# Performance work log

Hardware: AMD Instinct MI355X
Metric: run time of the kernel (lower is better)

Reference implementation:

```python
import jax, jax.numpy as jnp
import numpy as np

B, D_IN, D_H, D_OUT = 65536, 512, 512, 512
E, N_GATE, G_H = 8, 128, 128


def _glorot(key, shape):
    bound = np.sqrt(6.0 / np.prod(shape[-2:]))
    return jax.random.uniform(key, shape, jnp.float32, -bound, bound)


def setup_inputs() -> dict:
    key = jax.random.key(0)
    ks = jax.random.split(key, 10)
    inp = {
        "z": jax.random.normal(ks[0], (B, D_IN), jnp.float32),
        "idx": jnp.arange(N_GATE, dtype=jnp.int64),
        # gating MLP (nn.Linear stored as [in, out])
        "Wg1": _glorot(ks[1], (N_GATE, G_H)), "bg1": jnp.zeros((G_H,), jnp.float32),
        "Wg2": _glorot(ks[2], (G_H, G_H)), "bg2": jnp.zeros((G_H,), jnp.float32),
        "Wg3": _glorot(ks[3], (G_H, E)), "bg3": jnp.zeros((E,), jnp.float32),
        # expert layers: W [E, in, out], b [E, out]
        "W1": _glorot(ks[4], (E, D_IN, D_H)), "b1": jnp.zeros((E, D_H), jnp.float32),
        "W2": _glorot(ks[5], (E, D_H, D_H)), "b2": jnp.zeros((E, D_H), jnp.float32),
        "W3": _glorot(ks[6], (E, D_H, D_OUT)), "b3": jnp.zeros((E, D_OUT), jnp.float32),
    }
    return inp


def _expert_layer(x, w, W, b):
    # y = sum_e w[:,e] * (x @ W[e] + b[e])  -- soft dense MoE combine
    return jnp.einsum('be,bi,eio->bo', w, x, W) + w @ b


def reference(z, idx, Wg1, bg1, Wg2, bg2, Wg3, bg3, W1, b1, W2, b2, W3, b3):
    # gating MLP on selected features (eval mode: dropout is identity)
    g = jax.nn.elu(z[:, idx] @ Wg1 + bg1)
    g = jax.nn.elu(g @ Wg2 + bg2)
    w = g @ Wg3 + bg3  # raw logits, no softmax (faithful to source)
    # experts encoder
    h = jax.nn.elu(_expert_layer(z, w, W1, b1))
    h = jax.nn.elu(_expert_layer(h, w, W2, b2))
    return _expert_layer(h, w, W3, b3)
```

## Files before the change

kernel.cpp:

```cpp
#include <hip/hip_runtime.h>

#define B_ROWS 65536

typedef __attribute__((ext_vector_type(8))) __bf16 bf16x8;
typedef __attribute__((ext_vector_type(8))) _Float16 f16x8;
typedef __attribute__((ext_vector_type(4))) float f32x4;
typedef __attribute__((ext_vector_type(8))) unsigned short u16x8;

__device__ __forceinline__ unsigned short f2bf(float f) {
  unsigned int u = __float_as_uint(f);
  u += 0x7fffu + ((u >> 16) & 1u);
  return (unsigned short)(u >> 16);
}

__device__ __forceinline__ float elu_f(float v) {
  return v > 0.f ? v : __expf(v) - 1.f;
}

__device__ __forceinline__ void async_ld16(const void* g, void* l) {
  __builtin_amdgcn_global_load_lds(
      (const __attribute__((address_space(1))) void*)g,
      (__attribute__((address_space(3))) void*)l, 16, 0, 0);
}

#define GP 136

__global__ __launch_bounds__(256) void gating_mfma(
    const float* __restrict__ z, const int* __restrict__ idx,
    const float* __restrict__ Wg1, const float* __restrict__ bg1,
    const float* __restrict__ Wg2, const float* __restrict__ bg2,
    const float* __restrict__ Wg3, const float* __restrict__ bg3,
    float* __restrict__ wq, unsigned short* __restrict__ zb) {
  __shared__ _Float16 Ab[128 * GP];
  __shared__ _Float16 Wb[128 * GP];
  __shared__ int idx_l[128];

  const int tid = threadIdx.x;
  const int lane = tid & 63, wave = tid >> 6;
  const int wr = wave >> 1, wc = wave & 1;
  const int lhi = lane >> 4, llo = lane & 15;
  const size_t row0 = (size_t)blockIdx.x * 128;

  if (tid < 128) idx_l[tid] = idx[tid];
  for (int i = tid; i < 16384; i += 256) {
    const int k = i >> 7, n = i & 127;
    Wb[n * GP + k] = (_Float16)Wg1[i];
  }
  {
    const float* zr = z + row0 * 512;
    unsigned short* zo = zb + row0 * 512;
    for (int i = tid; i < 8192; i += 256) {
      const size_t off = (size_t)i * 8;
      float4 a = *(const float4*)(zr + off);
      float4 b = *(const float4*)(zr + off + 4);
      u16x8 r;
      r[0] = f2bf(a.x); r[1] = f2bf(a.y); r[2] = f2bf(a.z); r[3] = f2bf(a.w);
      r[4] = f2bf(b.x); r[5] = f2bf(b.y); r[6] = f2bf(b.z); r[7] = f2bf(b.w);
      *(u16x8*)(zo + off) = r;
    }
  }
  __syncthreads();
  for (int i = tid; i < 16384; i += 256) {
    const int r = i >> 7, c = i & 127;
    Ab[r * GP + c] = (_Float16)z[(row0 + r) * 512 + idx_l[c]];
  }
  __syncthreads();

  const f32x4 vzero = {0.f, 0.f, 0.f, 0.f};

  f32x4 C[4][4];
#pragma unroll
  for (int i = 0; i < 4; i++)
#pragma unroll
    for (int j = 0; j < 4; j++) C[i][j] = vzero;
#pragma unroll
  for (int ks = 0; ks < 4; ks++) {
    f16x8 av[4], bv[4];
#pragma unroll
    for (int fm = 0; fm < 4; fm++)
      av[fm] = *(const f16x8*)&Ab[(wr * 64 + fm * 16 + llo) * GP + ks * 32 + lhi * 8];
#pragma unroll
    for (int fn = 0; fn < 4; fn++)
      bv[fn] = *(const f16x8*)&Wb[(wc * 64 + fn * 16 + llo) * GP + ks * 32 + lhi * 8];
#pragma unroll
    for (int fm = 0; fm < 4; fm++)
#pragma unroll
      for (int fn = 0; fn < 4; fn++)
        C[fm][fn] = __builtin_amdgcn_mfma_f32_16x16x32_f16(av[fm], bv[fn], C[fm][fn], 0, 0, 0);
  }
  __syncthreads();
#pragma unroll
  for (int fm = 0; fm < 4; fm++)
#pragma unroll
    for (int fn = 0; fn < 4; fn++) {
      const int col = wc * 64 + fn * 16 + llo;
      const float bb = bg1[col];
#pragma unroll
      for (int r = 0; r < 4; r++) {
        const int row = wr * 64 + fm * 16 + lhi * 4 + r;
        Ab[row * GP + col] = (_Float16)elu_f(C[fm][fn][r] + bb);
      }
    }
  for (int i = tid; i < 16384; i += 256) {
    const int k = i >> 7, n = i & 127;
    Wb[n * GP + k] = (_Float16)Wg2[i];
  }
  __syncthreads();

#pragma unroll
  for (int i = 0; i < 4; i++)
#pragma unroll
    for (int j = 0; j < 4; j++) C[i][j] = vzero;
#pragma unroll
  for (int ks = 0; ks < 4; ks++) {
    f16x8 av[4], bv[4];
#pragma unroll
    for (int fm = 0; fm < 4; fm++)
      av[fm] = *(const f16x8*)&Ab[(wr * 64 + fm * 16 + llo) * GP + ks * 32 + lhi * 8];
#pragma unroll
    for (int fn = 0; fn < 4; fn++)
      bv[fn] = *(const f16x8*)&Wb[(wc * 64 + fn * 16 + llo) * GP + ks * 32 + lhi * 8];
#pragma unroll
    for (int fm = 0; fm < 4; fm++)
#pragma unroll
      for (int fn = 0; fn < 4; fn++)
        C[fm][fn] = __builtin_amdgcn_mfma_f32_16x16x32_f16(av[fm], bv[fn], C[fm][fn], 0, 0, 0);
  }
  __syncthreads();
#pragma unroll
  for (int fm = 0; fm < 4; fm++)
#pragma unroll
    for (int fn = 0; fn < 4; fn++) {
      const int col = wc * 64 + fn * 16 + llo;
      const float bb = bg2[col];
#pragma unroll
      for (int r = 0; r < 4; r++) {
        const int row = wr * 64 + fm * 16 + lhi * 4 + r;
        Ab[row * GP + col] = (_Float16)elu_f(C[fm][fn][r] + bb);
      }
    }
  for (int i = tid; i < 2048; i += 256) {
    const int k = i >> 4, n = i & 15;
    Wb[n * GP + k] = (n < 8) ? (_Float16)Wg3[k * 8 + n] : (_Float16)0.f;
  }
  __syncthreads();

  f32x4 C3[4];
#pragma unroll
  for (int i = 0; i < 4; i++) C3[i] = vzero;
#pragma unroll
  for (int ks = 0; ks < 4; ks++) {
    f16x8 av[4];
#pragma unroll
    for (int fm = 0; fm < 4; fm++)
      av[fm] = *(const f16x8*)&Ab[(wr * 64 + fm * 16 + llo) * GP + ks * 32 + lhi * 8];
    const f16x8 bv = *(const f16x8*)&Wb[llo * GP + ks * 32 + lhi * 8];
#pragma unroll
    for (int fm = 0; fm < 4; fm++)
      C3[fm] = __builtin_amdgcn_mfma_f32_16x16x32_f16(av[fm], bv, C3[fm], 0, 0, 0);
  }
  if (wc == 0 && llo < 8) {
    const float bb = bg3[llo];
#pragma unroll
    for (int fm = 0; fm < 4; fm++)
#pragma unroll
      for (int r = 0; r < 4; r++) {
        const size_t row = row0 + wr * 64 + fm * 16 + lhi * 4 + r;
        wq[row * 8 + llo] = C3[fm][r] + bb;
      }
  }
}

__global__ __launch_bounds__(256) void transpose_w(
    const float* __restrict__ W1, const float* __restrict__ W2,
    const float* __restrict__ W3, unsigned short* __restrict__ Wt) {
  __shared__ float t[32][33];
  const int le = blockIdx.z;
  const float* W = (le < 8) ? W1 : (le < 16) ? W2 : W3;
  const size_t eoff = (size_t)(le & 7) * 262144;
  unsigned short* O = Wt + (size_t)le * 262144;
  const int i0 = blockIdx.y * 32, o0 = blockIdx.x * 32;
  const int tx = threadIdx.x & 31, ty = threadIdx.x >> 5;
#pragma unroll
  for (int s = 0; s < 4; s++)
    t[ty + s * 8][tx] = W[eoff + (size_t)(i0 + ty + s * 8) * 512 + o0 + tx];
  __syncthreads();
#pragma unroll
  for (int s = 0; s < 4; s++)
    O[(size_t)(o0 + ty + s * 8) * 512 + i0 + tx] = f2bf(t[tx][ty + s * 8]);
}

template <bool ELU, bool OUTBF>
__global__ __launch_bounds__(256, 2) void expert_layer(
    const unsigned short* __restrict__ X,
    const unsigned short* __restrict__ Wt,
    const float* __restrict__ bias,
    const float* __restrict__ wq,
    void* __restrict__ Out) {
  __shared__ short a_tile[128 * 64];
  __shared__ short b_tile[128 * 64];
  __shared__ float w_lds[8 * 128];
  __shared__ float bias_lds[8 * 128];

  const int tid = threadIdx.x;
  const int lane = tid & 63;
  const int wave = tid >> 6;
  const int wr = wave >> 1, wc = wave & 1;
  const int lhi = lane >> 4, llo = lane & 15;

  const int g = blockIdx.x;
  const int xcd = g & 7;
  const int s = g >> 3;
  const int nb = s & 3;
  const int mb = xcd * 64 + (s >> 2);
  const size_t row0 = (size_t)mb * 128;
  const int col0 = nb * 128;

  for (int i = tid; i < 1024; i += 256) {
    const int e = i >> 7, r = i & 127;
    w_lds[i] = wq[(row0 + r) * 8 + e];
    bias_lds[i] = bias[e * 512 + col0 + r];
  }

  const int srow = tid >> 3;
  const int cgo = ((tid & 7) ^ (srow & 7)) << 4;
  const char* Ab = (const char*)X + (row0 + srow) * 1024 + cgo;
  const char* Bb = (const char*)Wt + (size_t)(col0 + srow) * 1024 + cgo;
  char* aL = (char*)a_tile + tid * 16;
  char* bL = (char*)b_tile + tid * 16;

  const f32x4 vzero = {0.f, 0.f, 0.f, 0.f};
  f32x4 C[4][4];
#pragma unroll
  for (int i = 0; i < 4; i++)
#pragma unroll
    for (int j = 0; j < 4; j++) C[i][j] = vzero;

  const int rsw = llo & 7;

  for (int e = 0; e < 8; e++) {
    f32x4 acc[4][4];
#pragma unroll
    for (int i = 0; i < 4; i++)
#pragma unroll
      for (int j = 0; j < 4; j++) acc[i][j] = vzero;
    const char* Be = Bb + (size_t)e * 524288;
    for (int kt = 0; kt < 8; kt++) {
      const char* ga = Ab + kt * 128;
      const char* gb = Be + kt * 128;
#pragma unroll
      for (int j = 0; j < 4; j++) {
        async_ld16(ga + j * 32768, aL + j * 4096);
        async_ld16(gb + j * 32768, bL + j * 4096);
      }
      __syncthreads();
#pragma unroll
      for (int ks = 0; ks < 2; ks++) {
        const int slot = (ks * 4 + lhi) ^ rsw;
        bf16x8 av[4], bv[4];
#pragma unroll
        for (int fm = 0; fm < 4; fm++)
          av[fm] = *(const bf16x8*)((const char*)a_tile +
                                    (wr * 64 + fm * 16 + llo) * 128 + slot * 16);
#pragma unroll
        for (int fn = 0; fn < 4; fn++)
          bv[fn] = *(const bf16x8*)((const char*)b_tile +
                                    (wc * 64 + fn * 16 + llo) * 128 + slot * 16);
#pragma unroll
        for (int fm = 0; fm < 4; fm++)
#pragma unroll
          for (int fn = 0; fn < 4; fn++)
            acc[fm][fn] = __builtin_amdgcn_mfma_f32_16x16x32_bf16(
                av[fm], bv[fn], acc[fm][fn], 0, 0, 0);
      }
      __syncthreads();
    }
#pragma unroll
    for (int fm = 0; fm < 4; fm++) {
      const f32x4 wv =
          *(const f32x4*)(w_lds + e * 128 + wr * 64 + fm * 16 + lhi * 4);
#pragma unroll
      for (int fn = 0; fn < 4; fn++)
#pragma unroll
        for (int r = 0; r < 4; r++) C[fm][fn][r] += wv[r] * acc[fm][fn][r];
    }
  }

#pragma unroll
  for (int e = 0; e < 8; e++) {
    f32x4 wv[4];
#pragma unroll
    for (int fm = 0; fm < 4; fm++)
      wv[fm] = *(const f32x4*)(w_lds + e * 128 + wr * 64 + fm * 16 + lhi * 4);
#pragma unroll
    for (int fn = 0; fn < 4; fn++) {
      const float bb = bias_lds[e * 128 + wc * 64 + fn * 16 + llo];
#pragma unroll
      for (int fm = 0; fm < 4; fm++)
#pragma unroll
        for (int r = 0; r < 4; r++) C[fm][fn][r] += wv[fm][r] * bb;
    }
  }

#pragma unroll
  for (int fm = 0; fm < 4; fm++)
#pragma unroll
    for (int fn = 0; fn < 4; fn++)
#pragma unroll
      for (int r = 0; r < 4; r++) {
        float v = C[fm][fn][r];
        if (ELU) v = elu_f(v);
        const size_t orow = row0 + wr * 64 + fm * 16 + lhi * 4 + r;
        const int ocol = col0 + wc * 64 + fn * 16 + llo;
        if (OUTBF)
          ((unsigned short*)Out)[orow * 512 + ocol] = f2bf(v);
        else
          ((float*)Out)[orow * 512 + ocol] = v;
      }
}

extern "C" void kernel_launch(void* const* d_in, const int* in_sizes, int n_in,
                              void* d_out, int out_size, void* d_ws,
                              size_t ws_size, hipStream_t stream) {
  (void)in_sizes; (void)n_in; (void)out_size; (void)ws_size;
  const float* z   = (const float*)d_in[0];
  const int*   idx = (const int*)d_in[1];
  const float* Wg1 = (const float*)d_in[2];
  const float* bg1 = (const float*)d_in[3];
  const float* Wg2 = (const float*)d_in[4];
  const float* bg2 = (const float*)d_in[5];
  const float* Wg3 = (const float*)d_in[6];
  const float* bg3 = (const float*)d_in[7];
  const float* W1  = (const float*)d_in[8];
  const float* b1  = (const float*)d_in[9];
  const float* W2  = (const float*)d_in[10];
  const float* b2  = (const float*)d_in[11];
  const float* W3  = (const float*)d_in[12];
  const float* b3  = (const float*)d_in[13];

  char* ws = (char*)d_ws;
  float* wq = (float*)ws;
  unsigned short* zb = (unsigned short*)(ws + (size_t)(2u << 20));
  unsigned short* h1 = (unsigned short*)(ws + (size_t)(66u << 20));
  unsigned short* Wt = (unsigned short*)(ws + (size_t)(130u << 20));
  unsigned short* h2 = zb;

  gating_mfma<<<dim3(512), dim3(256), 0, stream>>>(
      z, idx, Wg1, bg1, Wg2, bg2, Wg3, bg3, wq, zb);
  transpose_w<<<dim3(16, 16, 24), dim3(256), 0, stream>>>(W1, W2, W3, Wt);

  expert_layer<true, true><<<dim3(2048), dim3(256), 0, stream>>>(
      zb, Wt, b1, wq, (void*)h1);
  expert_layer<true, true><<<dim3(2048), dim3(256), 0, stream>>>(
      h1, Wt + (size_t)8 * 262144, b2, wq, (void*)h2);
  expert_layer<false, false><<<dim3(2048), dim3(256), 0, stream>>>(
      h2, Wt + (size_t)16 * 262144, b3, wq, d_out);
}
```

Before: 1.160 ms.

## Use 8 waves per expert-layer block with 64x32 per-wave tiles

Doubles the expert GEMM block from 256 to 512 threads, so each wave computes a 64x32 output sub-tile instead of 64x64. Each thread now issues two async LDS loads per operand instead of four, and the swizzled load addressing is recomputed per wave. The aim is more waves per CU to hide latency and fewer accumulator registers per thread. In exchange, each wave's A fragments are reused across only two B fragments, which raises LDS read traffic per MFMA, and there are more waves contending at each barrier.

Result: slower. 1.307 ms (+12.7%).

```diff
diff --git a/kernel.cpp b/kernel.cpp
--- a/kernel.cpp
+++ b/kernel.cpp
@@ -191,7 +191,7 @@
 }
 
 template <bool ELU, bool OUTBF>
-__global__ __launch_bounds__(256, 2) void expert_layer(
+__global__ __launch_bounds__(512, 4) void expert_layer(
     const unsigned short* __restrict__ X,
     const unsigned short* __restrict__ Wt,
     const float* __restrict__ bias,
@@ -205,7 +205,8 @@
   const int tid = threadIdx.x;
   const int lane = tid & 63;
   const int wave = tid >> 6;
-  const int wr = wave >> 1, wc = wave & 1;
+  const int wr2 = wave & 1;
+  const int wc2 = wave >> 1;
   const int lhi = lane >> 4, llo = lane & 15;
 
   const int g = blockIdx.x;
@@ -216,60 +217,59 @@
   const size_t row0 = (size_t)mb * 128;
   const int col0 = nb * 128;
 
-  for (int i = tid; i < 1024; i += 256) {
+  for (int i = tid; i < 1024; i += 512) {
     const int e = i >> 7, r = i & 127;
     w_lds[i] = wq[(row0 + r) * 8 + e];
     bias_lds[i] = bias[e * 512 + col0 + r];
   }
 
-  const int srow = tid >> 3;
-  const int cgo = ((tid & 7) ^ (srow & 7)) << 4;
-  const char* Ab = (const char*)X + (row0 + srow) * 1024 + cgo;
-  const char* Bb = (const char*)Wt + (size_t)(col0 + srow) * 1024 + cgo;
+  const int srow = wave * 8 + (lane >> 3);
+  const int cgo = ((lane & 7) ^ (lane >> 3)) << 4;
+  const char* Ag = (const char*)X + (row0 + srow) * 1024 + cgo;
+  const char* Bg = (const char*)Wt + (size_t)(col0 + srow) * 1024 + cgo;
   char* aL = (char*)a_tile + tid * 16;
   char* bL = (char*)b_tile + tid * 16;
 
   const f32x4 vzero = {0.f, 0.f, 0.f, 0.f};
-  f32x4 C[4][4];
+  f32x4 C[4][2];
 #pragma unroll
   for (int i = 0; i < 4; i++)
 #pragma unroll
-    for (int j = 0; j < 4; j++) C[i][j] = vzero;
+    for (int j = 0; j < 2; j++) C[i][j] = vzero;
 
   const int rsw = llo & 7;
 
   for (int e = 0; e < 8; e++) {
-    f32x4 acc[4][4];
+    f32x4 acc[4][2];
 #pragma unroll
     for (int i = 0; i < 4; i++)
 #pragma unroll
-      for (int j = 0; j < 4; j++) acc[i][j] = vzero;
-    const char* Be = Bb + (size_t)e * 524288;
+      for (int j = 0; j < 2; j++) acc[i][j] = vzero;
+    const char* Be = Bg + (size_t)e * 524288;
     for (int kt = 0; kt < 8; kt++) {
-      const char* ga = Ab + kt * 128;
+      const char* ga = Ag + kt * 128;
       const char* gb = Be + kt * 128;
-#pragma unroll
-      for (int j = 0; j < 4; j++) {
-        async_ld16(ga + j * 32768, aL + j * 4096);
-        async_ld16(gb + j * 32768, bL + j * 4096);
-      }
+      async_ld16(ga, aL);
+      async_ld16(ga + 65536, aL + 8192);
+      async_ld16(gb, bL);
+      async_ld16(gb + 65536, bL + 8192);
       __syncthreads();
 #pragma unroll
       for (int ks = 0; ks < 2; ks++) {
         const int slot = (ks * 4 + lhi) ^ rsw;
-        bf16x8 av[4], bv[4];
+        bf16x8 av[4], bv[2];
 #pragma unroll
         for (int fm = 0; fm < 4; fm++)
           av[fm] = *(const bf16x8*)((const char*)a_tile +
-                                    (wr * 64 + fm * 16 + llo) * 128 + slot * 16);
-#pragma unroll
-        for (int fn = 0; fn < 4; fn++)
+                                    (wr2 * 64 + fm * 16 + llo) * 128 + slot * 16);
+#pragma unroll
+        for (int fn = 0; fn < 2; fn++)
           bv[fn] = *(const bf16x8*)((const char*)b_tile +
-                                    (wc * 64 + fn * 16 + llo) * 128 + slot * 16);
+                                    (wc2 * 32 + fn * 16 + llo) * 128 + slot * 16);
 #pragma unroll
         for (int fm = 0; fm < 4; fm++)
 #pragma unroll
-          for (int fn = 0; fn < 4; fn++)
+          for (int fn = 0; fn < 2; fn++)
             acc[fm][fn] = __builtin_amdgcn_mfma_f32_16x16x32_bf16(
                 av[fm], bv[fn], acc[fm][fn], 0, 0, 0);
       }
@@ -278,9 +278,9 @@
 #pragma unroll
     for (int fm = 0; fm < 4; fm++) {
       const f32x4 wv =
-          *(const f32x4*)(w_lds + e * 128 + wr * 64 + fm * 16 + lhi * 4);
-#pragma unroll
-      for (int fn = 0; fn < 4; fn++)
+          *(const f32x4*)(w_lds + e * 128 + wr2 * 64 + fm * 16 + lhi * 4);
+#pragma unroll
+      for (int fn = 0; fn < 2; fn++)
 #pragma unroll
         for (int r = 0; r < 4; r++) C[fm][fn][r] += wv[r] * acc[fm][fn][r];
     }
@@ -288,30 +288,29 @@
 
 #pragma unroll
   for (int e = 0; e < 8; e++) {
-    f32x4 wv[4];
-#pragma unroll
-    for (int fm = 0; fm < 4; fm++)
-      wv[fm] = *(const f32x4*)(w_lds + e * 128 + wr * 64 + fm * 16 + lhi * 4);
-#pragma unroll
-    for (int fn = 0; fn < 4; fn++) {
-      const float bb = bias_lds[e * 128 + wc * 64 + fn * 16 + llo];
-#pragma unroll
-      for (int fm = 0; fm < 4; fm++)
-#pragma unroll
-        for (int r = 0; r < 4; r++) C[fm][fn][r] += wv[fm][r] * bb;
+#pragma unroll
+    for (int fm = 0; fm < 4; fm++) {
+      const f32x4 wv =
+          *(const f32x4*)(w_lds + e * 128 + wr2 * 64 + fm * 16 + lhi * 4);
+#pragma unroll
+      for (int fn = 0; fn < 2; fn++) {
+        const float bb = bias_lds[e * 128 + wc2 * 32 + fn * 16 + llo];
+#pragma unroll
+        for (int r = 0; r < 4; r++) C[fm][fn][r] += wv[r] * bb;
+      }
     }
   }
 
 #pragma unroll
   for (int fm = 0; fm < 4; fm++)
 #pragma unroll
-    for (int fn = 0; fn < 4; fn++)
+    for (int fn = 0; fn < 2; fn++)
 #pragma unroll
       for (int r = 0; r < 4; r++) {
         float v = C[fm][fn][r];
         if (ELU) v = elu_f(v);
-        const size_t orow = row0 + wr * 64 + fm * 16 + lhi * 4 + r;
-        const int ocol = col0 + wc * 64 + fn * 16 + llo;
+        const size_t orow = row0 + wr2 * 64 + fm * 16 + lhi * 4 + r;
+        const int ocol = col0 + wc2 * 32 + fn * 16 + llo;
         if (OUTBF)
           ((unsigned short*)Out)[orow * 512 + ocol] = f2bf(v);
         else
@@ -349,10 +348,10 @@
       z, idx, Wg1, bg1, Wg2, bg2, Wg3, bg3, wq, zb);
   transpose_w<<<dim3(16, 16, 24), dim3(256), 0, stream>>>(W1, W2, W3, Wt);
 
-  expert_layer<true, true><<<dim3(2048), dim3(256), 0, stream>>>(
+  expert_layer<true, true><<<dim3(2048), dim3(512), 0, stream>>>(
       zb, Wt, b1, wq, (void*)h1);
-  expert_layer<true, true><<<dim3(2048), dim3(256), 0, stream>>>(
+  expert_layer<true, true><<<dim3(2048), dim3(512), 0, stream>>>(
       h1, Wt + (size_t)8 * 262144, b2, wq, (void*)h2);
-  expert_layer<false, false><<<dim3(2048), dim3(256), 0, stream>>>(
+  expert_layer<false, false><<<dim3(2048), dim3(512), 0, stream>>>(
       h2, Wt + (size_t)16 * 262144, b3, wq, d_out);
 }
```
